# Performance work log

Measured on AMD Instinct MI355X. Metric: run time of the kernel, lower is better.

The kernel has to match this reference:

```python
import jax, jax.numpy as jnp
import numpy as np

INPUT_DIM = 1024
OUTPUT_DIM = 1024


def setup_inputs() -> dict:
    key = jax.random.key(0)
    k1, k2, k3, k4 = jax.random.split(key, 4)
    B, S, D = 4, 2048, INPUT_DIM
    src = jax.random.normal(k1, (B, S, D), dtype=jnp.float32)
    tgt = jax.random.normal(k2, (B, S, D), dtype=jnp.float32)
    # nn.Linear(input_dim*2, output_dim): weight [out, in], bias [out]
    bound = 1.0 / np.sqrt(2 * D)
    W = jax.random.uniform(k3, (OUTPUT_DIM, 2 * D), jnp.float32, -bound, bound)
    b = jax.random.uniform(k4, (OUTPUT_DIM,), jnp.float32, -bound, bound)
    return {"src": src, "tgt": tgt, "W": W, "b": b}


def reference(src, tgt, W, b):
    # weight = bmm(tgt, src^T): [B, S_tgt, S_src]
    weight = jnp.einsum("btd,bsd->bts", tgt, src)
    # NOTE: original uses Softmax(dim=1) -> normalizes over the tgt axis
    weight = jax.nn.softmax(weight, axis=1)
    # weighted sum over src positions: [B, S_tgt, D]
    weight_sum = jnp.einsum("bts,bsd->btd", weight, src)
    output = jnp.concatenate([weight_sum, tgt], axis=2)  # [B, S_tgt, 2D]
    output = output @ W.T + b  # [B, S_tgt, output_dim]
    return (output, weight)
```

## Files before the change

kernel.cpp:

```cpp
#include <hip/hip_runtime.h>
#include <stdint.h>


#define B_   4
#define S_   2048
#define D_   1024
#define OUTD 1024

typedef unsigned short ushort_t;
typedef _Float16 half8 __attribute__((ext_vector_type(8)));
typedef float    f32x4 __attribute__((ext_vector_type(4)));

__device__ __forceinline__ ushort_t f2h(float f) {
    union { _Float16 h; ushort_t u; } v;
    v.h = (_Float16)f;
    return v.u;
}
__device__ __forceinline__ float h2f(ushort_t u) {
    union { _Float16 h; ushort_t u; } v;
    v.u = u;
    return (float)v.h;
}

__device__ __forceinline__ void ld16(const ushort_t* g, ushort_t* l) {
    __builtin_amdgcn_global_load_lds(
        (const __attribute__((address_space(1))) void*)g,
        (__attribute__((address_space(3))) void*)l, 16, 0, 0);
}


__global__ void k_split(const float4* __restrict__ src, const float4* __restrict__ tgt,
                        const float4* __restrict__ W,
                        ushort4* __restrict__ sh,
                        ushort4* __restrict__ th, ushort4* __restrict__ tl,
                        ushort4* __restrict__ wb)
{
    const int64_t n4 = (int64_t)B_ * S_ * D_ / 4;
    const int64_t w4 = (int64_t)OUTD * 2 * D_ / 4;
    for (int64_t i = (int64_t)blockIdx.x * blockDim.x + threadIdx.x; i < n4 + w4;
         i += (int64_t)gridDim.x * blockDim.x) {
        if (i < n4) {
            float4 s = src[i];
            sh[i] = (ushort4){f2h(s.x), f2h(s.y), f2h(s.z), f2h(s.w)};
            float4 tv = tgt[i];
            ushort4 ht = {f2h(tv.x), f2h(tv.y), f2h(tv.z), f2h(tv.w)};
            th[i] = ht;
            tl[i] = (ushort4){f2h(tv.x - h2f(ht.x)), f2h(tv.y - h2f(ht.y)),
                              f2h(tv.z - h2f(ht.z)), f2h(tv.w - h2f(ht.w))};
        } else {
            int64_t j = i - n4;
            float4 w = W[j];
            wb[j] = (ushort4){f2h(w.x), f2h(w.y), f2h(w.z), f2h(w.w)};
        }
    }
}

__launch_bounds__(512, 2)
__global__ void k_gemm_logits(const ushort_t* __restrict__ Ah, const ushort_t* __restrict__ Al,
                              const ushort_t* __restrict__ Bs,
                              float* __restrict__ C,
                              float* __restrict__ pm, float* __restrict__ ps)
{
    const int M = S_, N = S_, K = D_;
    int wg = blockIdx.x + 8 * blockIdx.y + 64 * blockIdx.z;
    int bx = (wg >> 3) & 7;
    int g  = (wg & 7) + 8 * (wg >> 6);
    int by = g & 7;
    int b  = g >> 3;

    Ah += (int64_t)b * M * K;  Al += (int64_t)b * M * K;
    Bs += (int64_t)b * N * K;
    C  += (int64_t)b * M * N;

    __shared__ __align__(16) ushort_t lds[3 * 24576];
    __shared__ float red_m[2][256], red_s[2][256];

    int t    = threadIdx.x;
    int m0   = by * 256, n0 = bx * 256;
    int wave = t >> 6, lane = t & 63;
    int wr   = (wave >> 2) * 128;
    int wc   = (wave & 3) * 64;
    int l15  = lane & 15, quad = lane >> 4;

    f32x4 acc[8][4];
#pragma unroll
    for (int i = 0; i < 8; i++)
#pragma unroll
        for (int j = 0; j < 4; j++) acc[i][j] = (f32x4){0.f, 0.f, 0.f, 0.f};

    int pr   = t >> 3;
    int slot = t & 7;
    int cg   = slot ^ (pr & 7);
    int srow = pr * 2 + (cg >> 2);
    int scol = (cg & 3) * 8;

    const ushort_t* gAh = Ah + (int64_t)(m0 + srow) * K + scol;
    const ushort_t* gAl = Al + (int64_t)(m0 + srow) * K + scol;
    const ushort_t* gB  = Bs + (int64_t)(n0 + srow) * K + scol;
    const int64_t rstep = (int64_t)128 * K;

    auto stage_all = [&](int bufi, int kofs) {
        ushort_t* Lb = lds + bufi * 24576 + t * 8;
        ld16(gAh + kofs,         Lb);
        ld16(gAh + rstep + kofs, Lb + 4096);
        ld16(gAl + kofs,         Lb + 8192);
        ld16(gAl + rstep + kofs, Lb + 12288);
        ld16(gB  + kofs,         Lb + 16384);
        ld16(gB  + rstep + kofs, Lb + 20480);
    };

    int aoff[8], boff[4];
#pragma unroll
    for (int i = 0; i < 8; i++) {
        int R = wr + i * 16 + l15;
        int p = R >> 1, c = ((R & 1) << 2) + quad;
        aoff[i] = p * 64 + ((c ^ (p & 7)) << 3);
    }
#pragma unroll
    for (int j = 0; j < 4; j++) {
        int R = wc + j * 16 + l15;
        int p = R >> 1, c = ((R & 1) << 2) + quad;
        boff[j] = p * 64 + ((c ^ (p & 7)) << 3);
    }

    const int NT = 32;
    stage_all(0, 0);
    stage_all(1, 32);

    for (int kt = 0; kt < NT; ++kt) {
        const ushort_t* Lb = lds + (kt % 3) * 24576;
        ushort_t* Ld = lds + ((kt + 2) % 3) * 24576 + t * 8;
        const int nofs = (kt + 2) * 32;
        const bool pre = (kt + 2) < NT;

        if (kt + 1 < NT) {
            asm volatile("s_waitcnt vmcnt(6)" ::: "memory");
        } else {
            asm volatile("s_waitcnt vmcnt(0)" ::: "memory");
        }
        __builtin_amdgcn_s_barrier();
        asm volatile("" ::: "memory");
        __builtin_amdgcn_sched_barrier(0);

        half8 av[4], bf[4];

#pragma unroll
        for (int j = 0; j < 4; j++) bf[j] = *(const half8*)(Lb + 16384 + boff[j]);
#pragma unroll
        for (int i = 0; i < 4; i++) av[i] = *(const half8*)(Lb + aoff[i]);
        if (pre) { ld16(gAh + nofs, Ld);  ld16(gAh + rstep + nofs, Ld + 4096); }
        __builtin_amdgcn_s_barrier();
        __builtin_amdgcn_s_setprio(1);
#pragma unroll
        for (int i = 0; i < 4; i++)
#pragma unroll
            for (int j = 0; j < 4; j++)
                acc[i][j] = __builtin_amdgcn_mfma_f32_16x16x32_f16(av[i], bf[j], acc[i][j], 0, 0, 0);
        __builtin_amdgcn_s_setprio(0);
        __builtin_amdgcn_s_barrier();

#pragma unroll
        for (int i = 0; i < 4; i++) av[i] = *(const half8*)(Lb + 8192 + aoff[i]);
        if (pre) { ld16(gAl + nofs, Ld + 8192);  ld16(gAl + rstep + nofs, Ld + 12288); }
        __builtin_amdgcn_s_barrier();
        __builtin_amdgcn_s_setprio(1);
#pragma unroll
        for (int i = 0; i < 4; i++)
#pragma unroll
            for (int j = 0; j < 4; j++)
                acc[i][j] = __builtin_amdgcn_mfma_f32_16x16x32_f16(av[i], bf[j], acc[i][j], 0, 0, 0);
        __builtin_amdgcn_s_setprio(0);
        __builtin_amdgcn_s_barrier();

#pragma unroll
        for (int i = 0; i < 4; i++) av[i] = *(const half8*)(Lb + aoff[4 + i]);
        if (pre) { ld16(gB + nofs, Ld + 16384);  ld16(gB + rstep + nofs, Ld + 20480); }
        __builtin_amdgcn_s_barrier();
        __builtin_amdgcn_s_setprio(1);
#pragma unroll
        for (int i = 0; i < 4; i++)
#pragma unroll
            for (int j = 0; j < 4; j++)
                acc[4 + i][j] = __builtin_amdgcn_mfma_f32_16x16x32_f16(av[i], bf[j], acc[4 + i][j], 0, 0, 0);
        __builtin_amdgcn_s_setprio(0);
        __builtin_amdgcn_s_barrier();

#pragma unroll
        for (int i = 0; i < 4; i++) av[i] = *(const half8*)(Lb + 8192 + aoff[4 + i]);
        __builtin_amdgcn_s_barrier();
        __builtin_amdgcn_s_setprio(1);
#pragma unroll
        for (int i = 0; i < 4; i++)
#pragma unroll
            for (int j = 0; j < 4; j++)
                acc[4 + i][j] = __builtin_amdgcn_mfma_f32_16x16x32_f16(av[i], bf[j], acc[4 + i][j], 0, 0, 0);
        __builtin_amdgcn_s_setprio(0);
    }

#pragma unroll
    for (int i = 0; i < 8; i++) {
        int row_base = m0 + wr + i * 16 + quad * 4;
#pragma unroll
        for (int j = 0; j < 4; j++) {
            int col = n0 + wc + j * 16 + l15;
#pragma unroll
            for (int r = 0; r < 4; r++)
                C[(int64_t)(row_base + r) * N + col] = acc[i][j][r];
        }
    }

    int wrow = wave >> 2;
#pragma unroll
    for (int j = 0; j < 4; j++) {
        float m = -3.0e38f;
#pragma unroll
        for (int i = 0; i < 8; i++)
#pragma unroll
            for (int r = 0; r < 4; r++) m = fmaxf(m, acc[i][j][r]);
        float s = 0.f;
#pragma unroll
        for (int i = 0; i < 8; i++)
#pragma unroll
            for (int r = 0; r < 4; r++) s += __expf(acc[i][j][r] - m);
#pragma unroll
        for (int d = 16; d <= 32; d <<= 1) {
            float m2 = __shfl_xor(m, d, 64);
            float s2 = __shfl_xor(s, d, 64);
            float nm = fmaxf(m, m2);
            s = s * __expf(m - nm) + s2 * __expf(m2 - nm);
            m = nm;
        }
        if (lane < 16) {
            red_m[wrow][wc + j * 16 + l15] = m;
            red_s[wrow][wc + j * 16 + l15] = s;
        }
    }
    __syncthreads();
    if (t < 256) {
        float ma = red_m[0][t], mb = red_m[1][t];
        float sa = red_s[0][t], sb = red_s[1][t];
        float m = fmaxf(ma, mb);
        float s = sa * __expf(ma - m) + sb * __expf(mb - m);
        int idx = by * (B_ * S_) + b * S_ + n0 + t;
        pm[idx] = m;
        ps[idx] = s;
    }
}


__global__ void k_colstats2(const float* __restrict__ pm, const float* __restrict__ ps,
                            float* __restrict__ cmax, float* __restrict__ cinv)
{
    int i = blockIdx.x * 256 + threadIdx.x;
    float m = -3.0e38f;
#pragma unroll
    for (int c = 0; c < 8; c++) m = fmaxf(m, pm[c * (B_ * S_) + i]);
    float sum = 0.f;
#pragma unroll
    for (int c = 0; c < 8; c++) sum += ps[c * (B_ * S_) + i] * __expf(pm[c * (B_ * S_) + i] - m);
    cmax[i] = m;
    cinv[i] = 1.0f / sum;
}

__global__ void k_softmax_norm(float4* __restrict__ L, const float4* __restrict__ cmax4,
                               const float4* __restrict__ cinv4, ushort4* __restrict__ wbf)
{
    const int64_t n4 = (int64_t)B_ * S_ * S_ / 4;
    for (int64_t i = (int64_t)blockIdx.x * blockDim.x + threadIdx.x; i < n4;
         i += (int64_t)gridDim.x * blockDim.x) {
        int b  = (int)(i >> 20);
        int c4 = (int)(i & 511);
        float4 x  = L[i];
        float4 cm = cmax4[b * 512 + c4];
        float4 ci = cinv4[b * 512 + c4];
        f32x4 w;
        w.x = __expf(x.x - cm.x) * ci.x;
        w.y = __expf(x.y - cm.y) * ci.y;
        w.z = __expf(x.z - cm.z) * ci.z;
        w.w = __expf(x.w - cm.w) * ci.w;
        __builtin_nontemporal_store(w, (f32x4*)&L[i]);
        wbf[i] = (ushort4){f2h(w.x), f2h(w.y), f2h(w.z), f2h(w.w)};
    }
}

__launch_bounds__(512, 2)
__global__ void k_gemm_nt2(const ushort_t* __restrict__ A0, int lda0, int64_t bsA0,
                           const ushort_t* __restrict__ B0, int ldb0, int64_t bsB0,
                           ushort_t* __restrict__ C0, int ldc0, int64_t bsC0,
                           const ushort_t* __restrict__ A1, int lda1, int64_t bsA1,
                           const ushort_t* __restrict__ B1, int ldb1, int64_t bsB1,
                           ushort_t* __restrict__ C1, int ldc1, int64_t bsC1)
{
    const int K = D_;
    int id = blockIdx.x;
    const ushort_t *A, *Bm;
    ushort_t* C;
    int lda, ldb, ldc, bx, by;
    if (id < 256) {
        int g = (id & 7) + 8 * (id >> 7);
        bx = (id >> 3) & 15;
        by = g & 3;
        int b = g >> 2;
        A = A0 + (int64_t)b * bsA0;  Bm = B0 + (int64_t)b * bsB0;  C = C0 + (int64_t)b * bsC0;
        lda = lda0; ldb = ldb0; ldc = ldc0;
    } else {
        int i2 = id - 256;
        int g = (i2 & 7) + 8 * (i2 >> 6);
        bx = (i2 >> 3) & 7;
        by = g & 7;
        int b = g >> 3;
        A = A1 + (int64_t)b * bsA1;  Bm = B1 + (int64_t)b * bsB1;  C = C1 + (int64_t)b * bsC1;
        lda = lda1; ldb = ldb1; ldc = ldc1;
    }

    __shared__ __align__(16) ushort_t lds[3 * 24576];

    int t    = threadIdx.x;
    int m0   = by * 256, n0 = bx * 128;
    int wave = t >> 6, lane = t & 63;
    int wr   = (wave >> 1) * 64;
    int wc   = (wave & 1) * 64;
    int l15  = lane & 15, quad = lane >> 4;

    f32x4 acc[4][4];
#pragma unroll
    for (int i = 0; i < 4; i++)
#pragma unroll
        for (int j = 0; j < 4; j++) acc[i][j] = (f32x4){0.f, 0.f, 0.f, 0.f};

    int srow = t >> 3;
    int cg   = (t & 7) ^ (srow & 7);
    int scol = cg * 8;

    const ushort_t* gA = A  + (int64_t)(m0 + srow) * lda + scol;
    const ushort_t* gB = Bm + (int64_t)(n0 + srow) * ldb + scol;

    auto stage = [&](int bufi, int k0) {
        ushort_t* Lb = lds + bufi * 24576 + t * 8;
        ld16(gA + k0,                        Lb);
        ld16(gA + (int64_t)64  * lda + k0,   Lb + 4096);
        ld16(gA + (int64_t)128 * lda + k0,   Lb + 8192);
        ld16(gA + (int64_t)192 * lda + k0,   Lb + 12288);
        ld16(gB + k0,                        Lb + 16384);
        ld16(gB + (int64_t)64  * ldb + k0,   Lb + 20480);
    };

    int aoff[4][2], boff[4][2];
#pragma unroll
    for (int i = 0; i < 4; i++) {
        int R = wr + i * 16 + l15;
#pragma unroll
        for (int h = 0; h < 2; h++) {
            int c = quad + h * 4;
            aoff[i][h] = R * 64 + ((c ^ (R & 7)) << 3);
        }
    }
#pragma unroll
    for (int j = 0; j < 4; j++) {
        int R = wc + j * 16 + l15;
#pragma unroll
        for (int h = 0; h < 2; h++) {
            int c = quad + h * 4;
            boff[j][h] = 16384 + R * 64 + ((c ^ (R & 7)) << 3);
        }
    }

    const int NT = K >> 6;
    stage(0, 0);
    stage(1, 64);

    for (int kt = 0; kt < NT; ++kt) {
        const ushort_t* Lb = lds + (kt % 3) * 24576;
        ushort_t* Ld = lds + ((kt + 2) % 3) * 24576 + t * 8;
        const int nofs = (kt + 2) * 64;
        const bool pre = (kt + 2) < NT;

        if (kt + 1 < NT) {
            asm volatile("s_waitcnt vmcnt(6)" ::: "memory");
        } else {
            asm volatile("s_waitcnt vmcnt(0)" ::: "memory");
        }
        __builtin_amdgcn_s_barrier();
        asm volatile("" ::: "memory");
        __builtin_amdgcn_sched_barrier(0);

        half8 af[4], bf[4];

#pragma unroll
        for (int i = 0; i < 4; i++) af[i] = *(const half8*)(Lb + aoff[i][0]);
#pragma unroll
        for (int j = 0; j < 4; j++) bf[j] = *(const half8*)(Lb + boff[j][0]);
        if (pre) {
            ld16(gA + nofs,                      Ld);
            ld16(gA + (int64_t)64  * lda + nofs, Ld + 4096);
            ld16(gA + (int64_t)128 * lda + nofs, Ld + 8192);
        }
        __builtin_amdgcn_s_barrier();
        __builtin_amdgcn_s_setprio(1);
#pragma unroll
        for (int i = 0; i < 4; i++)
#pragma unroll
            for (int j = 0; j < 4; j++)
                acc[i][j] = __builtin_amdgcn_mfma_f32_16x16x32_f16(af[i], bf[j], acc[i][j], 0, 0, 0);
        __builtin_amdgcn_s_setprio(0);
        __builtin_amdgcn_s_barrier();

#pragma unroll
        for (int i = 0; i < 4; i++) af[i] = *(const half8*)(Lb + aoff[i][1]);
#pragma unroll
        for (int j = 0; j < 4; j++) bf[j] = *(const half8*)(Lb + boff[j][1]);
        if (pre) {
            ld16(gA + (int64_t)192 * lda + nofs, Ld + 12288);
            ld16(gB + nofs,                      Ld + 16384);
            ld16(gB + (int64_t)64  * ldb + nofs, Ld + 20480);
        }
        __builtin_amdgcn_s_barrier();
        __builtin_amdgcn_s_setprio(1);
#pragma unroll
        for (int i = 0; i < 4; i++)
#pragma unroll
            for (int j = 0; j < 4; j++)
                acc[i][j] = __builtin_amdgcn_mfma_f32_16x16x32_f16(af[i], bf[j], acc[i][j], 0, 0, 0);
        __builtin_amdgcn_s_setprio(0);
    }

#pragma unroll
    for (int i = 0; i < 4; i++) {
        int row_base = m0 + wr + i * 16 + quad * 4;
#pragma unroll
        for (int j = 0; j < 4; j++) {
            int col = n0 + wc + j * 16 + l15;
#pragma unroll
            for (int r = 0; r < 4; r++)
                C[(int64_t)(row_base + r) * ldc + col] = f2h(acc[i][j][r]);
        }
    }
}

__launch_bounds__(512, 2)
__global__ void k_gemm_final(const ushort_t* __restrict__ Wt, const ushort_t* __restrict__ PT,
                             const ushort_t* __restrict__ Q, const float* __restrict__ bias,
                             float* __restrict__ out)
{
    const int K = S_, N = OUTD;
    int wg = blockIdx.x + 8 * blockIdx.y + 64 * blockIdx.z;
    int bx = (wg >> 3) & 7;
    int g  = (wg & 7) + 8 * (wg >> 6);
    int by = g & 7;
    int b  = g >> 3;

    const ushort_t* A  = Wt + (int64_t)b * S_ * S_;
    const ushort_t* Bm = PT + (int64_t)b * OUTD * S_;
    const ushort_t* Qb = Q  + (int64_t)b * S_ * OUTD;
    float* Cb = out + (int64_t)b * S_ * OUTD;

    __shared__ __align__(16) ushort_t lds[3 * 24576];

    int t    = threadIdx.x;
    int m0   = by * 256, n0 = bx * 128;
    int wave = t >> 6, lane = t & 63;
    int wr   = (wave >> 1) * 64;
    int wc   = (wave & 1) * 64;
    int l15  = lane & 15, quad = lane >> 4;

    f32x4 acc[4][4];
#pragma unroll
    for (int i = 0; i < 4; i++)
#pragma unroll
        for (int j = 0; j < 4; j++) acc[i][j] = (f32x4){0.f, 0.f, 0.f, 0.f};

    int srow = t >> 3;
    int cg   = (t & 7) ^ (srow & 7);
    int scol = cg * 8;

    const ushort_t* gA = A  + (int64_t)(m0 + srow) * K + scol;
    const ushort_t* gB = Bm + (int64_t)(n0 + srow) * K + scol;

    auto stage = [&](int bufi, int k0) {
        ushort_t* Lb = lds + bufi * 24576 + t * 8;
        ld16(gA + k0,                      Lb);
        ld16(gA + (int64_t)64  * K + k0,   Lb + 4096);
        ld16(gA + (int64_t)128 * K + k0,   Lb + 8192);
        ld16(gA + (int64_t)192 * K + k0,   Lb + 12288);
        ld16(gB + k0,                      Lb + 16384);
        ld16(gB + (int64_t)64  * K + k0,   Lb + 20480);
    };

    int aoff[4][2], boff[4][2];
#pragma unroll
    for (int i = 0; i < 4; i++) {
        int R = wr + i * 16 + l15;
#pragma unroll
        for (int h = 0; h < 2; h++) {
            int c = quad + h * 4;
            aoff[i][h] = R * 64 + ((c ^ (R & 7)) << 3);
        }
    }
#pragma unroll
    for (int j = 0; j < 4; j++) {
        int R = wc + j * 16 + l15;
#pragma unroll
        for (int h = 0; h < 2; h++) {
            int c = quad + h * 4;
            boff[j][h] = 16384 + R * 64 + ((c ^ (R & 7)) << 3);
        }
    }

    const int NT = K >> 6;
    stage(0, 0);
    stage(1, 64);

    for (int kt = 0; kt < NT; ++kt) {
        const ushort_t* Lb = lds + (kt % 3) * 24576;
        ushort_t* Ld = lds + ((kt + 2) % 3) * 24576 + t * 8;
        const int nofs = (kt + 2) * 64;
        const bool pre = (kt + 2) < NT;

        if (kt + 1 < NT) {
            asm volatile("s_waitcnt vmcnt(6)" ::: "memory");
        } else {
            asm volatile("s_waitcnt vmcnt(0)" ::: "memory");
        }
        __builtin_amdgcn_s_barrier();
        asm volatile("" ::: "memory");
        __builtin_amdgcn_sched_barrier(0);

        half8 af[4], bf[4];

#pragma unroll
        for (int i = 0; i < 4; i++) af[i] = *(const half8*)(Lb + aoff[i][0]);
#pragma unroll
        for (int j = 0; j < 4; j++) bf[j] = *(const half8*)(Lb + boff[j][0]);
        if (pre) {
            ld16(gA + nofs,                    Ld);
            ld16(gA + (int64_t)64  * K + nofs, Ld + 4096);
            ld16(gA + (int64_t)128 * K + nofs, Ld + 8192);
        }
        __builtin_amdgcn_s_barrier();
        __builtin_amdgcn_s_setprio(1);
#pragma unroll
        for (int i = 0; i < 4; i++)
#pragma unroll
            for (int j = 0; j < 4; j++)
                acc[i][j] = __builtin_amdgcn_mfma_f32_16x16x32_f16(af[i], bf[j], acc[i][j], 0, 0, 0);
        __builtin_amdgcn_s_setprio(0);
        __builtin_amdgcn_s_barrier();

#pragma unroll
        for (int i = 0; i < 4; i++) af[i] = *(const half8*)(Lb + aoff[i][1]);
#pragma unroll
        for (int j = 0; j < 4; j++) bf[j] = *(const half8*)(Lb + boff[j][1]);
        if (pre) {
            ld16(gA + (int64_t)192 * K + nofs, Ld + 12288);
            ld16(gB + nofs,                    Ld + 16384);
            ld16(gB + (int64_t)64  * K + nofs, Ld + 20480);
        }
        __builtin_amdgcn_s_barrier();
        __builtin_amdgcn_s_setprio(1);
#pragma unroll
        for (int i = 0; i < 4; i++)
#pragma unroll
            for (int j = 0; j < 4; j++)
                acc[i][j] = __builtin_amdgcn_mfma_f32_16x16x32_f16(af[i], bf[j], acc[i][j], 0, 0, 0);
        __builtin_amdgcn_s_setprio(0);
    }

#pragma unroll
    for (int i = 0; i < 4; i++) {
        int row_base = m0 + wr + i * 16 + quad * 4;
#pragma unroll
        for (int j = 0; j < 4; j++) {
            int col = n0 + wc + j * 16 + l15;
            float bv = bias[col];
#pragma unroll
            for (int r = 0; r < 4; r++) {
                int64_t idx = (int64_t)(row_base + r) * N + col;
                float v = acc[i][j][r] + h2f(Qb[idx]) + bv;
                __builtin_nontemporal_store(v, &Cb[idx]);
            }
        }
    }
}


extern "C" void kernel_launch(void* const* d_in, const int* in_sizes, int n_in,
                              void* d_out, int out_size, void* d_ws, size_t ws_size,
                              hipStream_t stream)
{
    const float* src  = (const float*)d_in[0];
    const float* tgt  = (const float*)d_in[1];
    const float* W    = (const float*)d_in[2];
    const float* bias = (const float*)d_in[3];

    float* out = (float*)d_out;
    float* Lw  = out + (size_t)B_ * S_ * OUTD;

    char*  ws = (char*)d_ws;
    size_t o  = 0;
    auto take = [&](size_t bytes) -> char* {
        char* p = ws + o;
        o += (bytes + 255) & ~(size_t)255;
        return p;
    };
    const size_t ELEMS = (size_t)B_ * S_ * D_;
    ushort_t* sh   = (ushort_t*)take(ELEMS * 2);
    ushort_t* th   = (ushort_t*)take(ELEMS * 2);
    ushort_t* tl   = (ushort_t*)take(ELEMS * 2);
    ushort_t* wbf  = (ushort_t*)take((size_t)B_ * S_ * S_ * 2);
    ushort_t* wb   = (ushort_t*)take((size_t)OUTD * 2 * D_ * 2);
    ushort_t* PT   = (ushort_t*)take((size_t)B_ * OUTD * S_ * 2);
    ushort_t* Qb   = (ushort_t*)take((size_t)B_ * S_ * OUTD * 2);
    float*    pm   = (float*)take(16 * (size_t)B_ * S_ * 4);
    float*    ps   = (float*)take(16 * (size_t)B_ * S_ * 4);
    float*    cmax = (float*)take((size_t)B_ * S_ * 4);
    float*    cinv = (float*)take((size_t)B_ * S_ * 4);
    (void)ws_size; (void)in_sizes; (void)n_in; (void)out_size;

    k_split<<<dim3(2560), dim3(256), 0, stream>>>(
        (const float4*)src, (const float4*)tgt, (const float4*)W,
        (ushort4*)sh, (ushort4*)th, (ushort4*)tl, (ushort4*)wb);

    k_gemm_nt2<<<dim3(512), dim3(512), 0, stream>>>(
        wb, 2 * D_, 0,  sh, D_, (int64_t)S_ * D_,  PT, S_, (int64_t)OUTD * S_,
        th, D_, (int64_t)S_ * D_,  wb + D_, 2 * D_, 0,  Qb, OUTD, (int64_t)S_ * OUTD);

    k_gemm_logits<<<dim3(8, 8, 4), dim3(512), 0, stream>>>(th, tl, sh, Lw, pm, ps);

    k_colstats2<<<dim3(32), dim3(256), 0, stream>>>(pm, ps, cmax, cinv);
    k_softmax_norm<<<dim3(2048), dim3(256), 0, stream>>>((float4*)Lw, (const float4*)cmax,
                                                         (const float4*)cinv, (ushort4*)wbf);

    k_gemm_final<<<dim3(8, 8, 4), dim3(512), 0, stream>>>(wbf, PT, Qb, bias, out);
}
```

Baseline: 327.2 us.

## Enlarge nt2 GEMM tiles to 256x256 with K=32 stages and halve grid

```diff
diff --git a/kernel.cpp b/kernel.cpp
--- a/kernel.cpp
+++ b/kernel.cpp
@@ -296,87 +296,86 @@
     const ushort_t *A, *Bm;
     ushort_t* C;
     int lda, ldb, ldc, bx, by;
-    if (id < 256) {
-        int g = (id & 7) + 8 * (id >> 7);
-        bx = (id >> 3) & 15;
+    if (id < 128) {
+        int g = (id & 7) + 8 * (id >> 6);
+        bx = (id >> 3) & 7;
         by = g & 3;
         int b = g >> 2;
         A = A0 + (int64_t)b * bsA0;  Bm = B0 + (int64_t)b * bsB0;  C = C0 + (int64_t)b * bsC0;
         lda = lda0; ldb = ldb0; ldc = ldc0;
     } else {
-        int i2 = id - 256;
-        int g = (i2 & 7) + 8 * (i2 >> 6);
-        bx = (i2 >> 3) & 7;
+        int i2 = id - 128;
+        int g = (i2 & 7) + 8 * (i2 >> 5);
+        bx = (i2 >> 3) & 3;
         by = g & 7;
         int b = g >> 3;
         A = A1 + (int64_t)b * bsA1;  Bm = B1 + (int64_t)b * bsB1;  C = C1 + (int64_t)b * bsC1;
         lda = lda1; ldb = ldb1; ldc = ldc1;
     }
 
-    __shared__ __align__(16) ushort_t lds[3 * 24576];
+    __shared__ __align__(16) ushort_t lds[3 * 16384];
 
     int t    = threadIdx.x;
-    int m0   = by * 256, n0 = bx * 128;
+    int m0   = by * 256, n0 = bx * 256;
     int wave = t >> 6, lane = t & 63;
-    int wr   = (wave >> 1) * 64;
-    int wc   = (wave & 1) * 64;
+    int wr   = (wave >> 2) * 128;
+    int wc   = (wave & 3) * 64;
     int l15  = lane & 15, quad = lane >> 4;
 
-    f32x4 acc[4][4];
-#pragma unroll
-    for (int i = 0; i < 4; i++)
+    f32x4 acc[8][4];
+#pragma unroll
+    for (int i = 0; i < 8; i++)
 #pragma unroll
         for (int j = 0; j < 4; j++) acc[i][j] = (f32x4){0.f, 0.f, 0.f, 0.f};
 
-    int srow = t >> 3;
-    int cg   = (t & 7) ^ (srow & 7);
-    int scol = cg * 8;
+    int pr   = t >> 3;
+    int slot = t & 7;
+    int cg   = slot ^ (pr & 7);
+    int srow = pr * 2 + (cg >> 2);
+    int scol = (cg & 3) * 8;
 
     const ushort_t* gA = A  + (int64_t)(m0 + srow) * lda + scol;
     const ushort_t* gB = Bm + (int64_t)(n0 + srow) * ldb + scol;
-
-    auto stage = [&](int bufi, int k0) {
-        ushort_t* Lb = lds + bufi * 24576 + t * 8;
-        ld16(gA + k0,                        Lb);
-        ld16(gA + (int64_t)64  * lda + k0,   Lb + 4096);
-        ld16(gA + (int64_t)128 * lda + k0,   Lb + 8192);
-        ld16(gA + (int64_t)192 * lda + k0,   Lb + 12288);
-        ld16(gB + k0,                        Lb + 16384);
-        ld16(gB + (int64_t)64  * ldb + k0,   Lb + 20480);
+    const int64_t rstepA = (int64_t)128 * lda;
+    const int64_t rstepB = (int64_t)128 * ldb;
+
+    auto stageA = [&](int bufi, int kofs) {
+        ushort_t* Lb = lds + bufi * 16384 + t * 8;
+        ld16(gA + kofs,          Lb);
+        ld16(gA + rstepA + kofs, Lb + 4096);
     };
-
-    int aoff[4][2], boff[4][2];
-#pragma unroll
-    for (int i = 0; i < 4; i++) {
+    auto stageB = [&](int bufi, int kofs) {
+        ushort_t* Lb = lds + bufi * 16384 + t * 8;
+        ld16(gB + kofs,          Lb + 8192);
+        ld16(gB + rstepB + kofs, Lb + 12288);
+    };
+
+    int aoff[8], boff[4];
+#pragma unroll
+    for (int i = 0; i < 8; i++) {
         int R = wr + i * 16 + l15;
-#pragma unroll
-        for (int h = 0; h < 2; h++) {
-            int c = quad + h * 4;
-            aoff[i][h] = R * 64 + ((c ^ (R & 7)) << 3);
-        }
+        int p = R >> 1, c = ((R & 1) << 2) + quad;
+        aoff[i] = p * 64 + ((c ^ (p & 7)) << 3);
     }
 #pragma unroll
     for (int j = 0; j < 4; j++) {
         int R = wc + j * 16 + l15;
-#pragma unroll
-        for (int h = 0; h < 2; h++) {
-            int c = quad + h * 4;
-            boff[j][h] = 16384 + R * 64 + ((c ^ (R & 7)) << 3);
-        }
-    }
-
-    const int NT = K >> 6;
-    stage(0, 0);
-    stage(1, 64);
+        int p = R >> 1, c = ((R & 1) << 2) + quad;
+        boff[j] = p * 64 + ((c ^ (p & 7)) << 3);
+    }
+
+    const int NT = K >> 5;
+    stageA(0, 0);  stageB(0, 0);
+    stageA(1, 32); stageB(1, 32);
 
     for (int kt = 0; kt < NT; ++kt) {
-        const ushort_t* Lb = lds + (kt % 3) * 24576;
-        ushort_t* Ld = lds + ((kt + 2) % 3) * 24576 + t * 8;
-        const int nofs = (kt + 2) * 64;
+        const ushort_t* Lb = lds + (kt % 3) * 16384;
+        const int buf2 = (kt + 2) % 3;
+        const int nofs = (kt + 2) * 32;
         const bool pre = (kt + 2) < NT;
 
         if (kt + 1 < NT) {
-            asm volatile("s_waitcnt vmcnt(6)" ::: "memory");
+            asm volatile("s_waitcnt vmcnt(4)" ::: "memory");
         } else {
             asm volatile("s_waitcnt vmcnt(0)" ::: "memory");
         }
@@ -384,48 +383,38 @@
         asm volatile("" ::: "memory");
         __builtin_amdgcn_sched_barrier(0);
 
-        half8 af[4], bf[4];
-
-#pragma unroll
-        for (int i = 0; i < 4; i++) af[i] = *(const half8*)(Lb + aoff[i][0]);
-#pragma unroll
-        for (int j = 0; j < 4; j++) bf[j] = *(const half8*)(Lb + boff[j][0]);
-        if (pre) {
-            ld16(gA + nofs,                      Ld);
-            ld16(gA + (int64_t)64  * lda + nofs, Ld + 4096);
-            ld16(gA + (int64_t)128 * lda + nofs, Ld + 8192);
-        }
-        __builtin_amdgcn_s_barrier();
-        __builtin_amdgcn_s_setprio(1);
-#pragma unroll
-        for (int i = 0; i < 4; i++)
-#pragma unroll
-            for (int j = 0; j < 4; j++)
-                acc[i][j] = __builtin_amdgcn_mfma_f32_16x16x32_f16(af[i], bf[j], acc[i][j], 0, 0, 0);
-        __builtin_amdgcn_s_setprio(0);
-        __builtin_amdgcn_s_barrier();
-
-#pragma unroll
-        for (int i = 0; i < 4; i++) af[i] = *(const half8*)(Lb + aoff[i][1]);
-#pragma unroll
-        for (int j = 0; j < 4; j++) bf[j] = *(const half8*)(Lb + boff[j][1]);
-        if (pre) {
-            ld16(gA + (int64_t)192 * lda + nofs, Ld + 12288);
-            ld16(gB + nofs,                      Ld + 16384);
-            ld16(gB + (int64_t)64  * ldb + nofs, Ld + 20480);
-        }
-        __builtin_amdgcn_s_barrier();
-        __builtin_amdgcn_s_setprio(1);
-#pragma unroll
-        for (int i = 0; i < 4; i++)
-#pragma unroll
-            for (int j = 0; j < 4; j++)
-                acc[i][j] = __builtin_amdgcn_mfma_f32_16x16x32_f16(af[i], bf[j], acc[i][j], 0, 0, 0);
-        __builtin_amdgcn_s_setprio(0);
-    }
-
-#pragma unroll
-    for (int i = 0; i < 4; i++) {
+        half8 av[4], bf[4];
+
+#pragma unroll
+        for (int j = 0; j < 4; j++) bf[j] = *(const half8*)(Lb + 8192 + boff[j]);
+#pragma unroll
+        for (int i = 0; i < 4; i++) av[i] = *(const half8*)(Lb + aoff[i]);
+        if (pre) stageA(buf2, nofs);
+        __builtin_amdgcn_s_barrier();
+        __builtin_amdgcn_s_setprio(1);
+#pragma unroll
+        for (int i = 0; i < 4; i++)
+#pragma unroll
+            for (int j = 0; j < 4; j++)
+                acc[i][j] = __builtin_amdgcn_mfma_f32_16x16x32_f16(av[i], bf[j], acc[i][j], 0, 0, 0);
+        __builtin_amdgcn_s_setprio(0);
+        __builtin_amdgcn_s_barrier();
+
+#pragma unroll
+        for (int i = 0; i < 4; i++) av[i] = *(const half8*)(Lb + aoff[4 + i]);
+        if (pre) stageB(buf2, nofs);
+        __builtin_amdgcn_s_barrier();
+        __builtin_amdgcn_s_setprio(1);
+#pragma unroll
+        for (int i = 0; i < 4; i++)
+#pragma unroll
+            for (int j = 0; j < 4; j++)
+                acc[4 + i][j] = __builtin_amdgcn_mfma_f32_16x16x32_f16(av[i], bf[j], acc[4 + i][j], 0, 0, 0);
+        __builtin_amdgcn_s_setprio(0);
+    }
+
+#pragma unroll
+    for (int i = 0; i < 8; i++) {
         int row_base = m0 + wr + i * 16 + quad * 4;
 #pragma unroll
         for (int j = 0; j < 4; j++) {
@@ -620,7 +609,7 @@
         (const float4*)src, (const float4*)tgt, (const float4*)W,
         (ushort4*)sh, (ushort4*)th, (ushort4*)tl, (ushort4*)wb);
 
-    k_gemm_nt2<<<dim3(512), dim3(512), 0, stream>>>(
+    k_gemm_nt2<<<dim3(256), dim3(512), 0, stream>>>(
         wb, 2 * D_, 0,  sh, D_, (int64_t)S_ * D_,  PT, S_, (int64_t)OUTD * S_,
         th, D_, (int64_t)S_ * D_,  wb + D_, 2 * D_, 0,  Qb, OUTD, (int64_t)S_ * OUTD);
 
```

Result: no change. 324.4 us (-0.9%).
